# Optimization experiments

Measured on AMD Instinct MI355X. Metric: run time of the kernel, lower is better.

Reference implementation:

```python
import jax, jax.numpy as jnp
import numpy as np

B, N_TOK, C, M, H = 4, 2048, 256, 64, 8


def setup_inputs() -> dict:
    key = jax.random.key(0)
    ks = jax.random.split(key, 10)
    s = 0.02
    return {
        "x1": jax.random.normal(ks[0], (B, N_TOK, C), dtype=jnp.float32),
        "x2": jax.random.normal(ks[1], (B, N_TOK, C), dtype=jnp.float32),
        "cor": jax.random.normal(ks[2], (B, N_TOK, 3), dtype=jnp.float32),
        "Wq": jax.random.normal(ks[3], (C, C), dtype=jnp.float32) * s,
        "Wkv": jax.random.normal(ks[4], (C, 2 * C), dtype=jnp.float32) * s,
        "Wcor": jax.random.normal(ks[5], (3, M), dtype=jnp.float32) * s,
        "Wproj": jax.random.normal(ks[6], (C, C), dtype=jnp.float32) * s,
        "bproj": jnp.zeros((C,), dtype=jnp.float32),
        "Wm": jax.random.normal(ks[7], (M, M), dtype=jnp.float32) * s,
        "bm": jnp.zeros((M,), dtype=jnp.float32),
        "N": N_TOK,
    }


def reference(x1, x2, cor, Wq, Wkv, Wcor, Wproj, bproj, Wm, bm, N):
    B_, n, C_ = x1.shape
    Dh = C_ // H                      # head dim = 32
    scale = Dh ** (-0.5)
    # projections (no bias on q/kv/cor_embed, qkv_bias=False)
    q = (x1 @ Wq).reshape(B_, n, H, Dh).transpose(0, 2, 1, 3)          # [B,H,N,Dh]
    kv = (x2 @ Wkv).reshape(B_, n, 2, H, Dh)
    k = kv[:, :, 0].transpose(0, 2, 1, 3)                              # [B,H,N,Dh]
    v = kv[:, :, 1].transpose(0, 2, 1, 3)                              # [B,H,N,Dh]
    cor_embed_ = cor @ Wcor                                            # [B,N,M]
    Mh = cor_embed_.shape[-1] // H
    cor_embed = cor_embed_.reshape(B_, n, H, Mh).transpose(0, 2, 1, 3) # [B,H,N,Mh]
    # attention (mask=None path); weights reused for two value matmuls
    attn = jax.nn.softmax(jnp.einsum('bhnd,bhmd->bhnm', q, k) * scale, axis=-1)
    x = jnp.einsum('bhnm,bhmd->bnhd', attn, v).reshape(B_, n, C_)
    c_reverse = jnp.einsum('bhnm,bhmd->bnhd', attn, cor_embed).reshape(B_, n, -1)
    motion = (c_reverse - cor_embed_) @ Wm + bm
    x = x @ Wproj + bproj
    return (x, motion)
```

## Files before the change

### kernel.cpp

```cpp
#include <hip/hip_runtime.h>

#define B_ 4
#define NTOK 2048
#define CCH 256
#define HH 8
#define DH 32
#define MM 64
#define DV 48
#define ROWS (B_*NTOK)

typedef __bf16 bf16_t;
typedef bf16_t bf16x8 __attribute__((ext_vector_type(8)));
typedef float f32x4 __attribute__((ext_vector_type(4)));
typedef unsigned int u32x4 __attribute__((ext_vector_type(4)));
typedef unsigned short u16;

#define QSCALE (0.17677669529663687f * 1.44269504088896340f)

__device__ __forceinline__ u16 f2bf(float x) {
    unsigned u = __builtin_bit_cast(unsigned, x);
    return (u16)((u + 0x7FFFu + ((u >> 16) & 1u)) >> 16);
}
__device__ __forceinline__ unsigned cvt_pk(float lo, float hi) {
    unsigned r;
    asm("v_cvt_pk_bf16_f32 %0, %1, %2" : "=v"(r) : "v"(lo), "v"(hi));
    return r;
}
__device__ __forceinline__ f32x4 mfma16(bf16x8 a, bf16x8 b, f32x4 c) {
    return __builtin_amdgcn_mfma_f32_16x16x32_bf16(a, b, c, 0, 0, 0);
}
#if __has_builtin(__builtin_amdgcn_exp2f)
#define EXP2(x) __builtin_amdgcn_exp2f(x)
#else
#define EXP2(x) exp2f(x)
#endif

__device__ __forceinline__ bf16x8 exp_transpose(f32x4 s0, f32x4 s1) {
    unsigned W0 = cvt_pk(EXP2(s0[0]), EXP2(s0[1]));
    unsigned W1 = cvt_pk(EXP2(s0[2]), EXP2(s0[3]));
    unsigned W2 = cvt_pk(EXP2(s1[0]), EXP2(s1[1]));
    unsigned W3 = cvt_pk(EXP2(s1[2]), EXP2(s1[3]));
    asm("v_permlane32_swap_b32 %0, %1" : "+v"(W0), "+v"(W2));
    asm("v_permlane32_swap_b32 %0, %1" : "+v"(W1), "+v"(W3));
    asm("v_permlane16_swap_b32 %0, %1" : "+v"(W0), "+v"(W2));
    asm("v_permlane16_swap_b32 %0, %1" : "+v"(W1), "+v"(W3));
    u32x4 pw; pw[0] = W0; pw[1] = W1; pw[2] = W2; pw[3] = W3;
    return __builtin_bit_cast(bf16x8, pw);
}

__global__ __launch_bounds__(256) void prep_k(
    const float* __restrict__ x1, const float* __restrict__ x2,
    const float* __restrict__ Wq, const float* __restrict__ Wkv,
    const float* __restrict__ Wproj, const float* __restrict__ cor,
    const float* __restrict__ Wcor, const float* __restrict__ Wm,
    u16* __restrict__ x1b, u16* __restrict__ x2b,
    u16* __restrict__ Wqt, u16* __restrict__ Wkvt, u16* __restrict__ Wprojt,
    u16* __restrict__ Vt, float* __restrict__ G) {
    int bx = blockIdx.x, tid = threadIdx.x;
    if (bx < 2048) {
        const float* X = (bx < 1024) ? x1 : x2;
        u16* Xb = (bx < 1024) ? x1b : x2b;
        size_t i = (size_t)(bx & 1023) * 256 + tid;
        f32x4 a0 = *(const f32x4*)(X + i * 8);
        f32x4 a1 = *(const f32x4*)(X + i * 8 + 4);
        u32x4 w;
        w[0] = cvt_pk(a0[0], a0[1]);
        w[1] = cvt_pk(a0[2], a0[3]);
        w[2] = cvt_pk(a1[0], a1[1]);
        w[3] = cvt_pk(a1[2], a1[3]);
        *(u32x4*)(Xb + i * 8) = w;
    } else if (bx < 3072) {
        int r = bx - 2048;
        const float* W; u16* Wt; int N, base;
        if (r < 256)      { W = Wq;    Wt = Wqt;    N = 256; base = r; }
        else if (r < 768) { W = Wkv;   Wt = Wkvt;   N = 512; base = r - 256; }
        else              { W = Wproj; Wt = Wprojt; N = 256; base = r - 768; }
        int i = base * 256 + tid;
        int k = i / N, n = i - k * N;
        Wt[(size_t)n * 256 + k] = f2bf(W[i]);
    } else if (bx < 3104) {
        int bh = bx - 3072;
        int b2 = bh >> 3;
        for (int n = tid; n < NTOK; n += 256) {
            const float* cp = cor + ((size_t)b2 * NTOK + n) * 3;
            u16* vp = Vt + ((size_t)bh * DV + 32) * NTOK + n;
            vp[0]        = f2bf(cp[0]);
            vp[NTOK]     = f2bf(cp[1]);
            vp[2 * NTOK] = f2bf(cp[2]);
            vp[3 * NTOK] = (u16)0x3F80;
        }
    } else {
        int idx = (bx - 3104) * 256 + tid;
        int m = idx & 63, hj = idx >> 6;
        int hh = hj / 3, j = hj - 3 * hh;
        float acc = 0.f;
#pragma unroll
        for (int t = 0; t < 8; t++)
            acc += Wcor[j * 64 + hh * 8 + t] * Wm[(hh * 8 + t) * 64 + m];
        G[idx] = acc;
    }
}

__global__ __launch_bounds__(256, 4) void qkv_k(
    const u16* __restrict__ x1b, const u16* __restrict__ x2b,
    const u16* __restrict__ Wqt, const u16* __restrict__ Wkvt,
    u16* __restrict__ Qh, u16* __restrict__ Kh, u16* __restrict__ Vt) {
    int lane = threadIdx.x & 63, wave = threadIdx.x >> 6;
    int g = lane >> 4, q = lane & 15;
    int m0 = blockIdx.x * 64 + wave * 16;
    bool isq = blockIdx.y < 4;
    const u16* Ab = isq ? x1b : x2b;
    const u16* Bt = isq ? Wqt : Wkvt;
    int c0 = (isq ? blockIdx.y : blockIdx.y - 4) * 64;
    f32x4 acc[4] = {};
#pragma unroll
    for (int k0 = 0; k0 < CCH; k0 += 32) {
        bf16x8 af = *(const bf16x8*)(Ab + (size_t)(m0 + q) * CCH + k0 + g * 8);
#pragma unroll
        for (int t = 0; t < 4; t++) {
            bf16x8 bfr = *(const bf16x8*)(Bt + (size_t)(c0 + t * 16 + q) * CCH + k0 + g * 8);
            acc[t] = mfma16(af, bfr, acc[t]);
        }
    }
#pragma unroll
    for (int t = 0; t < 4; t++) {
#pragma unroll
        for (int r = 0; r < 4; r++) {
            int row = m0 + 4 * g + r;
            int c = c0 + t * 16 + q;
            float v = acc[t][r];
            int b = row >> 11, n = row & 2047;
            if (isq) {
                Qh[((size_t)(b * HH + (c >> 5)) * NTOK + n) * DH + (c & 31)] = f2bf(v * QSCALE);
            } else if (c < 256) {
                Kh[((size_t)(b * HH + (c >> 5)) * NTOK + n) * DH + (c & 31)] = f2bf(v);
            } else {
                int cc = c - 256;
                Vt[((size_t)(b * HH + (cc >> 5)) * DV + (cc & 31)) * NTOK + n] = f2bf(v);
            }
        }
    }
}

__global__ __launch_bounds__(256, 4) void gemm2_k(
    const u16* __restrict__ Ab, const u16* __restrict__ Bt,
    float* __restrict__ o_x, const float* __restrict__ bias) {
    int lane = threadIdx.x & 63, wave = threadIdx.x >> 6;
    int g = lane >> 4, q = lane & 15;
    int m0 = blockIdx.x * 64 + wave * 16;
    int c0 = blockIdx.y * 64;
    f32x4 acc[4] = {};
#pragma unroll
    for (int k0 = 0; k0 < CCH; k0 += 32) {
        bf16x8 af = *(const bf16x8*)(Ab + (size_t)(m0 + q) * CCH + k0 + g * 8);
#pragma unroll
        for (int t = 0; t < 4; t++) {
            bf16x8 bfr = *(const bf16x8*)(Bt + (size_t)(c0 + t * 16 + q) * CCH + k0 + g * 8);
            acc[t] = mfma16(af, bfr, acc[t]);
        }
    }
#pragma unroll
    for (int t = 0; t < 4; t++) {
#pragma unroll
        for (int r = 0; r < 4; r++) {
            int row = m0 + 4 * g + r;
            int c = c0 + t * 16 + q;
            o_x[(size_t)row * CCH + c] = acc[t][r] + bias[c];
        }
    }
}

__global__ __launch_bounds__(256, 2) void attn_k(
    const u16* __restrict__ Qh, const u16* __restrict__ Kh, const u16* __restrict__ Vt,
    u16* __restrict__ xpre, float* __restrict__ pc) {
    __shared__ __align__(16) float cb[4][3][64][12];
    int bh = blockIdx.x;
    int b = bh >> 3, h = bh & 7;
    int ks = threadIdx.x >> 6;
    int lane = threadIdx.x & 63;
    int g = lane >> 4, q = lane & 15;
    int qbase = blockIdx.y * 64;

    const u16* Qp = Qh + ((size_t)bh * NTOK + qbase + q) * DH + g * 8;
    bf16x8 qf0 = *(const bf16x8*)Qp;
    bf16x8 qf1 = *(const bf16x8*)(Qp + 16 * DH);
    bf16x8 qf2 = *(const bf16x8*)(Qp + 32 * DH);
    bf16x8 qf3 = *(const bf16x8*)(Qp + 48 * DH);

    const u16* kp = Kh + (size_t)bh * NTOK * DH + (size_t)(ks * 512 + q) * DH + g * 8;
    const u16* Vb = Vt + (size_t)bh * DV * NTOK + (size_t)q * NTOK + ks * 512 + g * 8;

    f32x4 acc00 = {}, acc01 = {}, acc02 = {}, acc10 = {}, acc11 = {}, acc12 = {};
    f32x4 acc20 = {}, acc21 = {}, acc22 = {}, acc30 = {}, acc31 = {}, acc32 = {};
    const f32x4 zacc = {0.f, 0.f, 0.f, 0.f};
    int voff = 0;

#pragma unroll 1
    for (int t = 0; t < 16; t++) {
        bf16x8 ka = *(const bf16x8*)(kp);
        bf16x8 kb = *(const bf16x8*)(kp + 16 * DH);
        kp += 32 * DH;
        bf16x8 va = *(const bf16x8*)(Vb + voff);
        bf16x8 vb = *(const bf16x8*)(Vb + 16 * NTOK + voff);
        bf16x8 vc = *(const bf16x8*)(Vb + 32 * NTOK + voff);
        voff += 32;
        {
            f32x4 s0 = mfma16(ka, qf0, zacc);
            f32x4 s1 = mfma16(kb, qf0, zacc);
            bf16x8 pf = exp_transpose(s0, s1);
            acc00 = mfma16(pf, va, acc00);
            acc01 = mfma16(pf, vb, acc01);
            acc02 = mfma16(pf, vc, acc02);
        }
        {
            f32x4 s0 = mfma16(ka, qf1, zacc);
            f32x4 s1 = mfma16(kb, qf1, zacc);
            bf16x8 pf = exp_transpose(s0, s1);
            acc10 = mfma16(pf, va, acc10);
            acc11 = mfma16(pf, vb, acc11);
            acc12 = mfma16(pf, vc, acc12);
        }
        {
            f32x4 s0 = mfma16(ka, qf2, zacc);
            f32x4 s1 = mfma16(kb, qf2, zacc);
            bf16x8 pf = exp_transpose(s0, s1);
            acc20 = mfma16(pf, va, acc20);
            acc21 = mfma16(pf, vb, acc21);
            acc22 = mfma16(pf, vc, acc22);
        }
        {
            f32x4 s0 = mfma16(ka, qf3, zacc);
            f32x4 s1 = mfma16(kb, qf3, zacc);
            bf16x8 pf = exp_transpose(s0, s1);
            acc30 = mfma16(pf, va, acc30);
            acc31 = mfma16(pf, vb, acc31);
            acc32 = mfma16(pf, vc, acc32);
        }
    }

#define ST3(dst, x, y, z) { *(f32x4*)(dst) = x; *(f32x4*)((dst) + 4) = y; *(f32x4*)((dst) + 8) = z; }
    {
        float* s0 = &cb[ks][0][lane][0];
        float* s1 = &cb[ks][1][lane][0];
        float* s2 = &cb[ks][2][lane][0];
        switch (ks) {
            case 0: ST3(s0, acc10, acc11, acc12) ST3(s1, acc20, acc21, acc22) ST3(s2, acc30, acc31, acc32) break;
            case 1: ST3(s0, acc20, acc21, acc22) ST3(s1, acc30, acc31, acc32) ST3(s2, acc00, acc01, acc02) break;
            case 2: ST3(s0, acc30, acc31, acc32) ST3(s1, acc00, acc01, acc02) ST3(s2, acc10, acc11, acc12) break;
            default: ST3(s0, acc00, acc01, acc02) ST3(s1, acc10, acc11, acc12) ST3(s2, acc20, acc21, acc22) break;
        }
    }
    __syncthreads();
    f32x4 A0, A1, A2;
    switch (ks) {
        case 0:  A0 = acc00; A1 = acc01; A2 = acc02; break;
        case 1:  A0 = acc10; A1 = acc11; A2 = acc12; break;
        case 2:  A0 = acc20; A1 = acc21; A2 = acc22; break;
        default: A0 = acc30; A1 = acc31; A2 = acc32; break;
    }
#pragma unroll
    for (int d = 1; d < 4; d++) {
        int s = (ks + d) & 3;
        int j = (ks - s - 1) & 3;
        const float* r = &cb[s][j][lane][0];
        A0 += *(const f32x4*)(r);
        A1 += *(const f32x4*)(r + 4);
        A2 += *(const f32x4*)(r + 8);
    }

    float inv[4];
#pragma unroll
    for (int r = 0; r < 4; r++) inv[r] = 1.0f / __shfl(A2[r], (lane & 48) | 3, 64);
#pragma unroll
    for (int r = 0; r < 4; r++) {
        size_t nrow = (size_t)b * NTOK + qbase + ks * 16 + 4 * g + r;
        u16* xp = xpre + nrow * CCH + h * DH;
        xp[q] = f2bf(A0[r] * inv[r]);
        xp[16 + q] = f2bf(A1[r] * inv[r]);
        if (q < 3) pc[nrow * 24 + h * 3 + q] = A2[r] * inv[r];
    }
}

__global__ __launch_bounds__(256) void motion_k(
    const float* __restrict__ pc, const float* __restrict__ cor,
    const float* __restrict__ G, const float* __restrict__ bm,
    float* __restrict__ out) {
    __shared__ float Gs[24][64];
    __shared__ float u[4][24];
    int tid = threadIdx.x;
    for (int i = tid; i < 1536; i += 256) Gs[i >> 6][i & 63] = G[i];
    size_t tok0 = (size_t)blockIdx.x * 4;
    if (tid < 96) {
        int tl = tid / 24, e = tid - tl * 24;
        int j = e % 3;
        size_t token = tok0 + tl;
        u[tl][e] = pc[token * 24 + e] - cor[token * 3 + j];
    }
    __syncthreads();
    int tl = tid >> 6, m = tid & 63;
    float v = bm[m];
#pragma unroll
    for (int e = 0; e < 24; e++) v += u[tl][e] * Gs[e][m];
    out[(tok0 + tl) * 64 + m] = v;
}

extern "C" void kernel_launch(void* const* d_in, const int* in_sizes, int n_in,
                              void* d_out, int out_size, void* d_ws, size_t ws_size,
                              hipStream_t stream) {
    const float* x1    = (const float*)d_in[0];
    const float* x2    = (const float*)d_in[1];
    const float* cor   = (const float*)d_in[2];
    const float* Wq    = (const float*)d_in[3];
    const float* Wkv   = (const float*)d_in[4];
    const float* Wcor  = (const float*)d_in[5];
    const float* Wproj = (const float*)d_in[6];
    const float* bproj = (const float*)d_in[7];
    const float* Wm    = (const float*)d_in[8];
    const float* bm    = (const float*)d_in[9];
    float* out_x = (float*)d_out;
    float* out_motion = out_x + (size_t)ROWS * CCH;

    u16* Wqt    = (u16*)d_ws;
    u16* Wkvt   = Wqt + 65536;
    u16* Wprojt = Wkvt + 131072;
    u16* x1b    = Wprojt + 65536;
    u16* x2b    = x1b + (size_t)2097152;
    u16* Qh     = x2b + (size_t)2097152;
    u16* Kh     = Qh + (size_t)2097152;
    u16* Vt     = Kh + (size_t)2097152;
    u16* xpre   = Vt + (size_t)3145728;
    float* pcb  = (float*)(xpre + (size_t)2097152);
    float* G    = pcb + (size_t)ROWS * 24;

    prep_k<<<3110, 256, 0, stream>>>(x1, x2, Wq, Wkv, Wproj, cor, Wcor, Wm,
                                     x1b, x2b, Wqt, Wkvt, Wprojt, Vt, G);
    qkv_k<<<dim3(128, 12), 256, 0, stream>>>(x1b, x2b, Wqt, Wkvt, Qh, Kh, Vt);
    attn_k<<<dim3(32, 32), 256, 0, stream>>>(Qh, Kh, Vt, xpre, pcb);
    gemm2_k<<<dim3(128, 4), 256, 0, stream>>>(xpre, Wprojt, out_x, bproj);
    motion_k<<<ROWS / 4, 256, 0, stream>>>(pcb, cor, G, bm, out_motion);
}
```

Before: 96.13 us.

## Fuse x1/x2 bf16 conversion into QKV GEMM and merge output kernels

Drops the separate fp32-to-bf16 conversion of x1/x2 from the prep kernel. The QKV GEMM now loads fp32 activations and converts them in registers. The output projection GEMM and the motion kernel are merged into one launch that selects its work by block index. This removes a full write and re-read of the bf16 activation copies and one kernel launch, at the cost of the QKV kernel reading twice as many bytes per A fragment, repeated across the 4-8 column blocks.

```diff
diff --git a/kernel.cpp b/kernel.cpp
--- a/kernel.cpp
+++ b/kernel.cpp
@@ -34,6 +34,17 @@
 #else
 #define EXP2(x) exp2f(x)
 #endif
+
+__device__ __forceinline__ bf16x8 ldcvt8(const float* p) {
+    f32x4 a0 = *(const f32x4*)p;
+    f32x4 a1 = *(const f32x4*)(p + 4);
+    u32x4 w;
+    w[0] = cvt_pk(a0[0], a0[1]);
+    w[1] = cvt_pk(a0[2], a0[3]);
+    w[2] = cvt_pk(a1[0], a1[1]);
+    w[3] = cvt_pk(a1[2], a1[3]);
+    return __builtin_bit_cast(bf16x8, w);
+}
 
 __device__ __forceinline__ bf16x8 exp_transpose(f32x4 s0, f32x4 s1) {
     unsigned W0 = cvt_pk(EXP2(s0[0]), EXP2(s0[1]));
@@ -49,37 +60,22 @@
 }
 
 __global__ __launch_bounds__(256) void prep_k(
-    const float* __restrict__ x1, const float* __restrict__ x2,
     const float* __restrict__ Wq, const float* __restrict__ Wkv,
     const float* __restrict__ Wproj, const float* __restrict__ cor,
     const float* __restrict__ Wcor, const float* __restrict__ Wm,
-    u16* __restrict__ x1b, u16* __restrict__ x2b,
     u16* __restrict__ Wqt, u16* __restrict__ Wkvt, u16* __restrict__ Wprojt,
     u16* __restrict__ Vt, float* __restrict__ G) {
     int bx = blockIdx.x, tid = threadIdx.x;
-    if (bx < 2048) {
-        const float* X = (bx < 1024) ? x1 : x2;
-        u16* Xb = (bx < 1024) ? x1b : x2b;
-        size_t i = (size_t)(bx & 1023) * 256 + tid;
-        f32x4 a0 = *(const f32x4*)(X + i * 8);
-        f32x4 a1 = *(const f32x4*)(X + i * 8 + 4);
-        u32x4 w;
-        w[0] = cvt_pk(a0[0], a0[1]);
-        w[1] = cvt_pk(a0[2], a0[3]);
-        w[2] = cvt_pk(a1[0], a1[1]);
-        w[3] = cvt_pk(a1[2], a1[3]);
-        *(u32x4*)(Xb + i * 8) = w;
-    } else if (bx < 3072) {
-        int r = bx - 2048;
+    if (bx < 1024) {
         const float* W; u16* Wt; int N, base;
-        if (r < 256)      { W = Wq;    Wt = Wqt;    N = 256; base = r; }
-        else if (r < 768) { W = Wkv;   Wt = Wkvt;   N = 512; base = r - 256; }
-        else              { W = Wproj; Wt = Wprojt; N = 256; base = r - 768; }
+        if (bx < 256)      { W = Wq;    Wt = Wqt;    N = 256; base = bx; }
+        else if (bx < 768) { W = Wkv;   Wt = Wkvt;   N = 512; base = bx - 256; }
+        else               { W = Wproj; Wt = Wprojt; N = 256; base = bx - 768; }
         int i = base * 256 + tid;
         int k = i / N, n = i - k * N;
         Wt[(size_t)n * 256 + k] = f2bf(W[i]);
-    } else if (bx < 3104) {
-        int bh = bx - 3072;
+    } else if (bx < 1056) {
+        int bh = bx - 1024;
         int b2 = bh >> 3;
         for (int n = tid; n < NTOK; n += 256) {
             const float* cp = cor + ((size_t)b2 * NTOK + n) * 3;
@@ -90,7 +86,7 @@
             vp[3 * NTOK] = (u16)0x3F80;
         }
     } else {
-        int idx = (bx - 3104) * 256 + tid;
+        int idx = (bx - 1056) * 256 + tid;
         int m = idx & 63, hj = idx >> 6;
         int hh = hj / 3, j = hj - 3 * hh;
         float acc = 0.f;
@@ -102,20 +98,20 @@
 }
 
 __global__ __launch_bounds__(256, 4) void qkv_k(
-    const u16* __restrict__ x1b, const u16* __restrict__ x2b,
+    const float* __restrict__ x1, const float* __restrict__ x2,
     const u16* __restrict__ Wqt, const u16* __restrict__ Wkvt,
     u16* __restrict__ Qh, u16* __restrict__ Kh, u16* __restrict__ Vt) {
     int lane = threadIdx.x & 63, wave = threadIdx.x >> 6;
     int g = lane >> 4, q = lane & 15;
     int m0 = blockIdx.x * 64 + wave * 16;
     bool isq = blockIdx.y < 4;
-    const u16* Ab = isq ? x1b : x2b;
+    const float* X = isq ? x1 : x2;
     const u16* Bt = isq ? Wqt : Wkvt;
     int c0 = (isq ? blockIdx.y : blockIdx.y - 4) * 64;
     f32x4 acc[4] = {};
 #pragma unroll
     for (int k0 = 0; k0 < CCH; k0 += 32) {
-        bf16x8 af = *(const bf16x8*)(Ab + (size_t)(m0 + q) * CCH + k0 + g * 8);
+        bf16x8 af = ldcvt8(X + (size_t)(m0 + q) * CCH + k0 + g * 8);
 #pragma unroll
         for (int t = 0; t < 4; t++) {
             bf16x8 bfr = *(const bf16x8*)(Bt + (size_t)(c0 + t * 16 + q) * CCH + k0 + g * 8);
@@ -138,34 +134,6 @@
                 int cc = c - 256;
                 Vt[((size_t)(b * HH + (cc >> 5)) * DV + (cc & 31)) * NTOK + n] = f2bf(v);
             }
-        }
-    }
-}
-
-__global__ __launch_bounds__(256, 4) void gemm2_k(
-    const u16* __restrict__ Ab, const u16* __restrict__ Bt,
-    float* __restrict__ o_x, const float* __restrict__ bias) {
-    int lane = threadIdx.x & 63, wave = threadIdx.x >> 6;
-    int g = lane >> 4, q = lane & 15;
-    int m0 = blockIdx.x * 64 + wave * 16;
-    int c0 = blockIdx.y * 64;
-    f32x4 acc[4] = {};
-#pragma unroll
-    for (int k0 = 0; k0 < CCH; k0 += 32) {
-        bf16x8 af = *(const bf16x8*)(Ab + (size_t)(m0 + q) * CCH + k0 + g * 8);
-#pragma unroll
-        for (int t = 0; t < 4; t++) {
-            bf16x8 bfr = *(const bf16x8*)(Bt + (size_t)(c0 + t * 16 + q) * CCH + k0 + g * 8);
-            acc[t] = mfma16(af, bfr, acc[t]);
-        }
-    }
-#pragma unroll
-    for (int t = 0; t < 4; t++) {
-#pragma unroll
-        for (int r = 0; r < 4; r++) {
-            int row = m0 + 4 * g + r;
-            int c = c0 + t * 16 + q;
-            o_x[(size_t)row * CCH + c] = acc[t][r] + bias[c];
         }
     }
 }
@@ -281,27 +249,56 @@
     }
 }
 
-__global__ __launch_bounds__(256) void motion_k(
-    const float* __restrict__ pc, const float* __restrict__ cor,
-    const float* __restrict__ G, const float* __restrict__ bm,
-    float* __restrict__ out) {
+__global__ __launch_bounds__(256) void out_k(
+    const u16* __restrict__ xpre, const u16* __restrict__ Wprojt,
+    const float* __restrict__ bias, const float* __restrict__ pc,
+    const float* __restrict__ cor, const float* __restrict__ G,
+    const float* __restrict__ bm, float* __restrict__ o_x,
+    float* __restrict__ o_m) {
     __shared__ float Gs[24][64];
     __shared__ float u[4][24];
     int tid = threadIdx.x;
-    for (int i = tid; i < 1536; i += 256) Gs[i >> 6][i & 63] = G[i];
-    size_t tok0 = (size_t)blockIdx.x * 4;
-    if (tid < 96) {
-        int tl = tid / 24, e = tid - tl * 24;
-        int j = e % 3;
-        size_t token = tok0 + tl;
-        u[tl][e] = pc[token * 24 + e] - cor[token * 3 + j];
-    }
-    __syncthreads();
-    int tl = tid >> 6, m = tid & 63;
-    float v = bm[m];
-#pragma unroll
-    for (int e = 0; e < 24; e++) v += u[tl][e] * Gs[e][m];
-    out[(tok0 + tl) * 64 + m] = v;
+    if (blockIdx.x < 512) {
+        int bx = blockIdx.x;
+        int lane = tid & 63, wave = tid >> 6;
+        int g = lane >> 4, q = lane & 15;
+        int m0 = (bx >> 2) * 64 + wave * 16;
+        int c0 = (bx & 3) * 64;
+        f32x4 acc[4] = {};
+#pragma unroll
+        for (int k0 = 0; k0 < CCH; k0 += 32) {
+            bf16x8 af = *(const bf16x8*)(xpre + (size_t)(m0 + q) * CCH + k0 + g * 8);
+#pragma unroll
+            for (int t = 0; t < 4; t++) {
+                bf16x8 bfr = *(const bf16x8*)(Wprojt + (size_t)(c0 + t * 16 + q) * CCH + k0 + g * 8);
+                acc[t] = mfma16(af, bfr, acc[t]);
+            }
+        }
+#pragma unroll
+        for (int t = 0; t < 4; t++) {
+#pragma unroll
+            for (int r = 0; r < 4; r++) {
+                int row = m0 + 4 * g + r;
+                int c = c0 + t * 16 + q;
+                o_x[(size_t)row * CCH + c] = acc[t][r] + bias[c];
+            }
+        }
+    } else {
+        for (int i = tid; i < 1536; i += 256) Gs[i >> 6][i & 63] = G[i];
+        size_t tok0 = (size_t)(blockIdx.x - 512) * 4;
+        if (tid < 96) {
+            int tl = tid / 24, e = tid - tl * 24;
+            int j = e % 3;
+            size_t token = tok0 + tl;
+            u[tl][e] = pc[token * 24 + e] - cor[token * 3 + j];
+        }
+        __syncthreads();
+        int tl = tid >> 6, m = tid & 63;
+        float v = bm[m];
+#pragma unroll
+        for (int e = 0; e < 24; e++) v += u[tl][e] * Gs[e][m];
+        o_m[(tok0 + tl) * 64 + m] = v;
+    }
 }
 
 extern "C" void kernel_launch(void* const* d_in, const int* in_sizes, int n_in,
@@ -323,19 +320,17 @@
     u16* Wqt    = (u16*)d_ws;
     u16* Wkvt   = Wqt + 65536;
     u16* Wprojt = Wkvt + 131072;
-    u16* x1b    = Wprojt + 65536;
-    u16* x2b    = x1b + (size_t)2097152;
-    u16* Qh     = x2b + (size_t)2097152;
+    u16* Qh     = Wprojt + 65536;
     u16* Kh     = Qh + (size_t)2097152;
     u16* Vt     = Kh + (size_t)2097152;
     u16* xpre   = Vt + (size_t)3145728;
     float* pcb  = (float*)(xpre + (size_t)2097152);
     float* G    = pcb + (size_t)ROWS * 24;
 
-    prep_k<<<3110, 256, 0, stream>>>(x1, x2, Wq, Wkv, Wproj, cor, Wcor, Wm,
-                                     x1b, x2b, Wqt, Wkvt, Wprojt, Vt, G);
-    qkv_k<<<dim3(128, 12), 256, 0, stream>>>(x1b, x2b, Wqt, Wkvt, Qh, Kh, Vt);
+    prep_k<<<1062, 256, 0, stream>>>(Wq, Wkv, Wproj, cor, Wcor, Wm,
+                                     Wqt, Wkvt, Wprojt, Vt, G);
+    qkv_k<<<dim3(128, 12), 256, 0, stream>>>(x1, x2, Wqt, Wkvt, Qh, Kh, Vt);
     attn_k<<<dim3(32, 32), 256, 0, stream>>>(Qh, Kh, Vt, xpre, pcb);
-    gemm2_k<<<dim3(128, 4), 256, 0, stream>>>(xpre, Wprojt, out_x, bproj);
-    motion_k<<<ROWS / 4, 256, 0, stream>>>(pcb, cor, G, bm, out_motion);
-}
+    out_k<<<2560, 256, 0, stream>>>(xpre, Wprojt, bproj, pcb, cor, G, bm,
+                                    out_x, out_motion);
+}
```

Measured after the change: 98.07 us. +2.0%, slower.
